# Performance work log

Hardware: AMD Instinct MI355X
Metric: run time of the kernel (lower is better)

Reference implementation:

```python
import math
import jax, jax.numpy as jnp
import numpy as np

B, T, C = 4, 2048, 1024
N_HEAD = 16
HEAD_DIM = C // N_HEAD


def setup_inputs() -> dict:
    key = jax.random.key(0)
    k1, k2, k3 = jax.random.split(key, 3)
    x = jax.random.normal(k1, (B, T, C), dtype=jnp.float32)
    # nn.Linear weights: (out_features, in_features); init scale ~1/sqrt(C)
    w_attn = jax.random.normal(k2, (3 * C, C), dtype=jnp.float32) / math.sqrt(C)
    w_proj = jax.random.normal(k3, (C, C), dtype=jnp.float32) / math.sqrt(C)
    return {"x": x, "w_attn": w_attn, "w_proj": w_proj}


def reference(x, w_attn, w_proj):
    Bx, Tx, Cx = x.shape
    qkv = x @ w_attn.T  # (B,T,3C)
    q, k, v = jnp.split(qkv, 3, axis=2)
    # (B,T,H,D) -> (B,H,T,D)
    q = q.reshape(Bx, Tx, N_HEAD, HEAD_DIM).transpose(0, 2, 1, 3)
    k = k.reshape(Bx, Tx, N_HEAD, HEAD_DIM).transpose(0, 2, 1, 3)
    v = v.reshape(Bx, Tx, N_HEAD, HEAD_DIM).transpose(0, 2, 1, 3)
    scale = 1.0 / math.sqrt(HEAD_DIM)
    att = jnp.einsum("bhqd,bhkd->bhqk", q, k) * scale
    causal = jnp.tril(jnp.ones((Tx, Tx), dtype=bool))
    att = jnp.where(causal[None, None, :, :], att, -jnp.inf)
    att = jax.nn.softmax(att, axis=-1)
    out = jnp.einsum("bhqk,bhkd->bhqd", att, v)
    out = out.transpose(0, 2, 1, 3).reshape(Bx, Tx, Cx)
    return out @ w_proj.T
```

## Files before the change

### kernel.cpp

```cpp
#include <hip/hip_runtime.h>
#include <hip/hip_bf16.h>


typedef __attribute__((ext_vector_type(8))) short bf16x8;
typedef __attribute__((ext_vector_type(4))) float f32x4;
typedef unsigned short ushort_t;

#if __has_builtin(__builtin_amdgcn_exp2f)
#define EXP2(x) __builtin_amdgcn_exp2f(x)
#else
#define EXP2(x) exp2f(x)
#endif

__device__ inline ushort_t f2bf(float f) {
    union { float f; unsigned int u; } x; x.f = f;
    return (ushort_t)((x.u + 0x7fffu + ((x.u >> 16) & 1u)) >> 16);
}

__device__ inline ushort_t f2bf_fast(float f) {
    union { float f; unsigned int u; } x; x.f = f;
    return (ushort_t)((x.u + 0x8000u) >> 16);
}

__device__ inline bf16x8 load8_f32_to_bf16(const float* p) {
    float4 f0 = *(const float4*)p;
    float4 f1 = *(const float4*)(p + 4);
    bf16x8 r;
    r[0] = (short)f2bf(f0.x); r[1] = (short)f2bf(f0.y);
    r[2] = (short)f2bf(f0.z); r[3] = (short)f2bf(f0.w);
    r[4] = (short)f2bf(f1.x); r[5] = (short)f2bf(f1.y);
    r[6] = (short)f2bf(f1.z); r[7] = (short)f2bf(f1.w);
    return r;
}

__device__ inline void gl2lds16(const ushort_t* g, ushort_t* l) {
    __builtin_amdgcn_global_load_lds(
        (const __attribute__((address_space(1))) unsigned int*)g,
        (__attribute__((address_space(3))) unsigned int*)l,
        16, 0, 0);
}

__global__ void cvt3(const float* __restrict__ a, long n8a,
                     const float* __restrict__ b, long n8b,
                     const float* __restrict__ c, long n8c,
                     ushort_t* __restrict__ out) {
    long i = (long)blockIdx.x * 256 + threadIdx.x;
    const float* src; long off;
    if (i < n8a) { src = a; off = i; }
    else if (i < n8a + n8b) { src = b; off = i - n8a; }
    else if (i < n8a + n8b + n8c) { src = c; off = i - n8a - n8b; }
    else return;
    *(bf16x8*)(out + i * 8) = load8_f32_to_bf16(src + off * 8);
}

__global__ void fill_zero_f32(float* out, int n) {
    int i = blockIdx.x * 256 + threadIdx.x;
    if (i < n) out[i] = 0.0f;
}

#define QK_LOG2E_SCALE 0.18033688011112042f

#define OVBUF 16384

template <int EPI>
__global__ __launch_bounds__(256) void gemm_ov(
        const ushort_t* __restrict__ A, const ushort_t* __restrict__ B,
        void* __restrict__ Cp, void* __restrict__ Cp2,
        int M, int N, int K) {
    __shared__ ushort_t S[2 * OVBUF];

    const int tid  = threadIdx.x;
    const int lane = tid & 63;
    const int w    = tid >> 6;
    const int quad = lane >> 4;
    const int l16  = lane & 15;
    const int wm   = (w & 1) * 64;
    const int wn   = (w >> 1) * 64;

    const int xcd = (int)blockIdx.x & 7;
    const int c   = (int)blockIdx.x >> 3;
    const int g   = c >> 6;
    const int ml  = (c >> 3) & 7;
    const int nl  = c & 7;
    const int bm  = ((xcd << 3) + ml) << 7;
    const int bn  = ((g << 3) + nl) << 7;

    const int nt = K >> 6;

    const int srow = lane >> 3;
    const int soct = (lane & 7) ^ srow;
    const ushort_t* Ag = A + (size_t)(bm + w * 32 + srow) * K + soct * 8;
    const ushort_t* Bg = B + (size_t)(bn + w * 32 + srow) * K + soct * 8;

    auto stage = [&](int kt) {
        ushort_t* d = S + (kt & 1) * OVBUF;
        const size_t ko = (size_t)kt * 64;
#pragma unroll
        for (int j = 0; j < 4; j++) {
            gl2lds16(Ag + ko + (size_t)(j * 8) * K, d + w * 2048 + j * 512);
            gl2lds16(Bg + ko + (size_t)(j * 8) * K, d + 8192 + w * 2048 + j * 512);
        }
    };

    const int sl7 = l16 & 7;
    const int ca0 = ((quad)     ^ sl7) * 8;
    const int ca1 = ((quad + 4) ^ sl7) * 8;
    const int arow = (wm + l16) * 64;
    const int brow = 8192 + (wn + l16) * 64;

    f32x4 acc[4][4] = {};

    stage(0);
    __asm__ __volatile__("s_waitcnt vmcnt(0)" ::: "memory");
    __builtin_amdgcn_s_barrier();

    for (int kt = 0; kt < nt; kt++) {
        if (kt + 1 < nt) stage(kt + 1);

        const ushort_t* Sb = S + (kt & 1) * OVBUF;
        bf16x8 af[4][2], bfr[4][2];
#pragma unroll
        for (int mi = 0; mi < 4; mi++) {
            af[mi][0] = *(const bf16x8*)(Sb + arow + mi * 1024 + ca0);
            af[mi][1] = *(const bf16x8*)(Sb + arow + mi * 1024 + ca1);
        }
#pragma unroll
        for (int ni = 0; ni < 4; ni++) {
            bfr[ni][0] = *(const bf16x8*)(Sb + brow + ni * 1024 + ca0);
            bfr[ni][1] = *(const bf16x8*)(Sb + brow + ni * 1024 + ca1);
        }

        __builtin_amdgcn_s_setprio(1);
#pragma unroll
        for (int mi = 0; mi < 4; mi++)
#pragma unroll
            for (int ni = 0; ni < 4; ni++)
#pragma unroll
                for (int kk = 0; kk < 2; kk++)
                    acc[mi][ni] = __builtin_amdgcn_mfma_f32_16x16x32_bf16(
                        af[mi][kk], bfr[ni][kk], acc[mi][ni], 0, 0, 0);
        __builtin_amdgcn_s_setprio(0);

        __asm__ __volatile__("s_waitcnt vmcnt(0)" ::: "memory");
        __builtin_amdgcn_s_barrier();
    }

    const int colbase = bn + wn;
    const int rowbase = bm + wm + quad * 4;
    if constexpr (EPI == 1) {
#pragma unroll
        for (int mi = 0; mi < 4; mi++) {
            const int row = rowbase + mi * 16;
            float* cr = (float*)Cp + (size_t)row * N + colbase + l16;
#pragma unroll
            for (int r = 0; r < 4; r++)
#pragma unroll
                for (int ni = 0; ni < 4; ni++)
                    cr[(size_t)r * N + ni * 16] = acc[mi][ni][r];
        }
    } else {
        if (colbase < 2048) {
            const float qs = (colbase < 1024) ? QK_LOG2E_SCALE : 1.0f;
#pragma unroll
            for (int mi = 0; mi < 4; mi++) {
                const int row = rowbase + mi * 16;
                ushort_t* qp = (ushort_t*)Cp + (size_t)row * 2048 + colbase + l16;
#pragma unroll
                for (int r = 0; r < 4; r++)
#pragma unroll
                    for (int ni = 0; ni < 4; ni++)
                        qp[(size_t)r * 2048 + ni * 16] = f2bf(acc[mi][ni][r] * qs);
            }
        } else {
#pragma unroll
            for (int mi = 0; mi < 4; mi++) {
                const int row = rowbase + mi * 16;
                const int bb = row >> 11, tt = row & 2047;
#pragma unroll
                for (int ni = 0; ni < 4; ni++) {
                    const int vc = colbase + ni * 16 + l16 - 2048;
                    const int hh = vc >> 6, dd = vc & 63;
                    ushort_t* vp = (ushort_t*)Cp2 +
                        ((((size_t)bb * 16 + hh) * 64 + dd) * 2048) + tt;
#pragma unroll
                    for (int r = 0; r < 4; r++)
                        vp[r] = f2bf(acc[mi][ni][r]);
                }
            }
        }
    }
}

#define BM 128
#define BN 128
#define BK 64
#define LDK 72

template <bool A_F32, bool B_F32, int EPI>
__global__ __launch_bounds__(256) void gemm_nt(
        const void* __restrict__ Ap, const void* __restrict__ Bp,
        void* __restrict__ Cp, void* __restrict__ Cp2,
        int M, int N, int K) {
    __shared__ ushort_t As[BM * LDK];
    __shared__ ushort_t Bs[BN * LDK];

    const int tid  = threadIdx.x;
    const int lane = tid & 63;
    const int w    = tid >> 6;
    const int quad = lane >> 4;
    const int l16  = lane & 15;

    const int bm = blockIdx.y * BM;
    const int bn = blockIdx.x * BN;
    const int wm = (w & 1) * 64;
    const int wn = (w >> 1) * 64;

    f32x4 acc[4][4] = {};

    const int lrow = tid >> 3;
    const int lcol = (tid & 7) * 8;

    bf16x8 pa[4], pb[4];
#pragma unroll
    for (int i = 0; i < 4; i++) {
        const int ra = lrow + i * 32;
        if constexpr (A_F32)
            pa[i] = load8_f32_to_bf16((const float*)Ap + (size_t)(bm + ra) * K + lcol);
        else
            pa[i] = *(const bf16x8*)((const ushort_t*)Ap + (size_t)(bm + ra) * K + lcol);
        if constexpr (B_F32)
            pb[i] = load8_f32_to_bf16((const float*)Bp + (size_t)(bn + ra) * K + lcol);
        else
            pb[i] = *(const bf16x8*)((const ushort_t*)Bp + (size_t)(bn + ra) * K + lcol);
    }

    for (int k0 = 0; k0 < K; k0 += BK) {
        __syncthreads();
#pragma unroll
        for (int i = 0; i < 4; i++) {
            *(bf16x8*)&As[(lrow + i * 32) * LDK + lcol] = pa[i];
            *(bf16x8*)&Bs[(lrow + i * 32) * LDK + lcol] = pb[i];
        }
        __syncthreads();

        if (k0 + BK < K) {
            const int kn = k0 + BK + lcol;
#pragma unroll
            for (int i = 0; i < 4; i++) {
                const int ra = lrow + i * 32;
                if constexpr (A_F32)
                    pa[i] = load8_f32_to_bf16((const float*)Ap + (size_t)(bm + ra) * K + kn);
                else
                    pa[i] = *(const bf16x8*)((const ushort_t*)Ap + (size_t)(bm + ra) * K + kn);
                if constexpr (B_F32)
                    pb[i] = load8_f32_to_bf16((const float*)Bp + (size_t)(bn + ra) * K + kn);
                else
                    pb[i] = *(const bf16x8*)((const ushort_t*)Bp + (size_t)(bn + ra) * K + kn);
            }
        }

#pragma unroll
        for (int ks = 0; ks < BK; ks += 32) {
            bf16x8 af[4], bfr[4];
#pragma unroll
            for (int i = 0; i < 4; i++)
                af[i] = *(const bf16x8*)&As[(wm + i * 16 + l16) * LDK + ks + quad * 8];
#pragma unroll
            for (int i = 0; i < 4; i++)
                bfr[i] = *(const bf16x8*)&Bs[(wn + i * 16 + l16) * LDK + ks + quad * 8];
#pragma unroll
            for (int mi = 0; mi < 4; mi++)
#pragma unroll
                for (int ni = 0; ni < 4; ni++)
                    acc[mi][ni] = __builtin_amdgcn_mfma_f32_16x16x32_bf16(
                        af[mi], bfr[ni], acc[mi][ni], 0, 0, 0);
        }
    }

#pragma unroll
    for (int mi = 0; mi < 4; mi++) {
        const int row0 = bm + wm + mi * 16 + quad * 4;
#pragma unroll
        for (int r = 0; r < 4; r++) {
            const int row = row0 + r;
            if constexpr (EPI == 1) {
                float* crow = (float*)Cp + (size_t)row * N + bn + wn;
#pragma unroll
                for (int ni = 0; ni < 4; ni++)
                    crow[ni * 16 + l16] = acc[mi][ni][r];
            } else {
                if (bn < 2048) {
                    const float qs = (bn < 1024) ? QK_LOG2E_SCALE : 1.0f;
                    ushort_t* crow = (ushort_t*)Cp + (size_t)row * 2048 + bn + wn;
#pragma unroll
                    for (int ni = 0; ni < 4; ni++)
                        crow[ni * 16 + l16] = f2bf(acc[mi][ni][r] * qs);
                } else {
                    ushort_t* vt = (ushort_t*)Cp2;
                    const int bb = row >> 11, tt = row & 2047;
#pragma unroll
                    for (int ni = 0; ni < 4; ni++) {
                        const int vc = bn + wn + ni * 16 + l16 - 2048;
                        const int hh = vc >> 6, dd = vc & 63;
                        vt[(((size_t)bb * 16 + hh) * 64 + dd) * 2048 + tt] =
                            f2bf(acc[mi][ni][r]);
                    }
                }
            }
        }
    }
}

#define AT_T 2048

__global__ __launch_bounds__(256) void attn4(
        const ushort_t* __restrict__ qk,
        const ushort_t* __restrict__ vt,
        ushort_t* __restrict__ attout) {
    const int bh   = blockIdx.x;
    const int ya   = (int)blockIdx.y >> 2;
    const int yr   = (int)blockIdx.y & 3;
    const int qblk = (ya == 0) ? 15 - yr
                   : (ya == 1) ? 8 + yr
                   : (ya == 2) ? 4 + yr
                   :             3 - yr;
    const int b    = bh >> 4;
    const int h    = bh & 15;

    const int tid  = threadIdx.x;
    const int lane = tid & 63;
    const int w    = tid >> 6;
    const int quad = lane >> 4;
    const int l16  = lane & 15;
    const int sw   = l16 & 7;

    __shared__ ushort_t Ks[64 * 64];
    __shared__ ushort_t Vs[64 * 64];
    __shared__ ushort_t Ps[4][32 * 64];

    bf16x8 vones;
#pragma unroll
    for (int j = 0; j < 8; j++) vones[j] = (short)0x3F80;

    const ushort_t* qp = qk + (size_t)b * AT_T * 2048 + h * 64;
    const ushort_t* kp = qp + 1024;
    const ushort_t* vp = vt + (size_t)bh * 64 * 2048;

    const int Q0 = qblk * 128 + w * 16;

    bf16x8 aq[2][2];
#pragma unroll
    for (int s = 0; s < 2; s++) {
        const ushort_t* qrow = qp + (size_t)(Q0 + s * 64 + l16) * 2048;
        aq[s][0] = *(const bf16x8*)(qrow + quad * 8);
        aq[s][1] = *(const bf16x8*)(qrow + 32 + quad * 8);
    }

    f32x4 o[2][5] = {};

    const int lr8 = lane >> 3;
    const int cbg = ((lane & 7) ^ lr8) * 8;

    const int nk = 2 * qblk + 2;
    for (int kt = 0; kt < nk; kt++) {
        const int k0 = kt * 64;
        if (kt) __syncthreads();
#pragma unroll
        for (int j = 0; j < 2; j++) {
            gl2lds16(kp + (size_t)(k0 + w * 16 + j * 8 + lr8) * 2048 + cbg,
                     &Ks[(w * 16 + j * 8) * 64]);
            gl2lds16(vp + (size_t)(w * 16 + j * 8 + lr8) * 2048 + k0 + cbg,
                     &Vs[(w * 16 + j * 8) * 64]);
        }
        __syncthreads();

        f32x4 s0[4], s1[4];
#pragma unroll
        for (int c = 0; c < 4; c++) {
            s0[c][0] = -8.0f; s0[c][1] = -8.0f; s0[c][2] = -8.0f; s0[c][3] = -8.0f;
            s1[c] = s0[c];
#pragma unroll
            for (int ks = 0; ks < 2; ks++) {
                const int cs = ((quad + 4 * ks) ^ sw) * 8;
                bf16x8 bk = *(const bf16x8*)&Ks[(c * 16 + l16) * 64 + cs];
                s0[c] = __builtin_amdgcn_mfma_f32_16x16x32_bf16(aq[0][ks], bk, s0[c], 0, 0, 0);
                s1[c] = __builtin_amdgcn_mfma_f32_16x16x32_bf16(aq[1][ks], bk, s1[c], 0, 0, 0);
            }
        }

        if (kt >= 2 * qblk) {
            const int q0r = Q0 + quad * 4;
#pragma unroll
            for (int c = 0; c < 4; c++) {
                const int kcol = k0 + c * 16 + l16;
#pragma unroll
                for (int r = 0; r < 4; r++)
                    if (kcol > q0r + r) s0[c][r] = -__builtin_inff();
            }
        }
        if (kt == 2 * qblk + 1) {
            const int q1r = Q0 + 64 + quad * 4;
#pragma unroll
            for (int c = 0; c < 4; c++) {
                const int kcol = k0 + c * 16 + l16;
#pragma unroll
                for (int r = 0; r < 4; r++)
                    if (kcol > q1r + r) s1[c][r] = -__builtin_inff();
            }
        }

#pragma unroll
        for (int c = 0; c < 4; c++)
#pragma unroll
            for (int r = 0; r < 4; r++) {
                const int row = quad * 4 + r;
                const int sidx = (((c * 2 + (l16 >> 3)) ^ (row & 7)) << 3) | sw;
                Ps[w][row * 64 + sidx]        = f2bf_fast(EXP2(s0[c][r]));
                Ps[w][(16 + row) * 64 + sidx] = f2bf_fast(EXP2(s1[c][r]));
            }

        __asm__ __volatile__("s_waitcnt lgkmcnt(0)" ::: "memory");

#pragma unroll
        for (int ks = 0; ks < 2; ks++) {
            const int cs = ((quad + 4 * ks) ^ sw) * 8;
            const int pslot = (((ks * 4 + quad) ^ sw) << 3);
            bf16x8 ap0 = *(const bf16x8*)&Ps[w][l16 * 64 + pslot];
            bf16x8 ap1 = *(const bf16x8*)&Ps[w][(16 + l16) * 64 + pslot];
#pragma unroll
            for (int n = 0; n < 4; n++) {
                bf16x8 bv = *(const bf16x8*)&Vs[(n * 16 + l16) * 64 + cs];
                o[0][n] = __builtin_amdgcn_mfma_f32_16x16x32_bf16(ap0, bv, o[0][n], 0, 0, 0);
                o[1][n] = __builtin_amdgcn_mfma_f32_16x16x32_bf16(ap1, bv, o[1][n], 0, 0, 0);
            }
            o[0][4] = __builtin_amdgcn_mfma_f32_16x16x32_bf16(ap0, vones, o[0][4], 0, 0, 0);
            o[1][4] = __builtin_amdgcn_mfma_f32_16x16x32_bf16(ap1, vones, o[1][4], 0, 0, 0);
        }
    }

#pragma unroll
    for (int s = 0; s < 2; s++) {
        ushort_t* op = attout + (size_t)(b * AT_T + Q0 + s * 64 + quad * 4) * 1024 + h * 64;
#pragma unroll
        for (int r = 0; r < 4; r++) {
            const float l = __shfl(o[s][4][r], lane & 48, 64);
            const float inv = 1.0f / fmaxf(l, 1e-30f);
            ushort_t* orow = op + (size_t)r * 1024;
#pragma unroll
            for (int n = 0; n < 4; n++)
                orow[n * 16 + l16] = f2bf(o[s][n][r] * inv);
        }
    }
}

extern "C" void kernel_launch(void* const* d_in, const int* in_sizes, int n_in,
                              void* d_out, int out_size, void* d_ws, size_t ws_size,
                              hipStream_t stream) {
    const float* x      = (const float*)d_in[0];
    const float* w_attn = (const float*)d_in[1];
    const float* w_proj = (const float*)d_in[2];
    float* out = (float*)d_out;

    const int M = 8192, C = 1024;
    const size_t E_QK  = (size_t)M * 2048;
    const size_t E_VT  = (size_t)4 * 16 * 64 * 2048;
    const size_t E_ATT = (size_t)M * 1024;
    const size_t E_X   = (size_t)M * 1024;
    const size_t E_WA  = (size_t)3072 * 1024;
    const size_t E_WP  = (size_t)1024 * 1024;
    const size_t need_mid  = (E_QK + E_VT + E_ATT) * 2;
    const size_t need_full = need_mid + (E_X + E_WA + E_WP) * 2;

    if (ws_size < need_mid) {
        fill_zero_f32<<<(out_size + 255) / 256, 256, 0, stream>>>(out, out_size);
        return;
    }

    ushort_t* qk  = (ushort_t*)d_ws;
    ushort_t* vt  = qk + E_QK;
    ushort_t* att = vt + E_VT;

    if (ws_size >= need_full) {
        ushort_t* xb  = att + E_ATT;
        const long n8x = (long)(E_X / 8), n8a = (long)(E_WA / 8), n8p = (long)(E_WP / 8);
        const long n8  = n8x + n8a + n8p;
        cvt3<<<(int)((n8 + 255) / 256), 256, 0, stream>>>(
            x, n8x, w_attn, n8a, w_proj, n8p, xb);

        ushort_t* wab = xb + E_X;
        ushort_t* wpb = wab + E_WA;
        gemm_ov<2><<<dim3((M / 128) * (3 * C / 128)), 256, 0, stream>>>(
            xb, wab, qk, vt, M, 3 * C, C);
        attn4<<<dim3(64, 16), 256, 0, stream>>>(qk, vt, att);
        gemm_ov<1><<<dim3((M / 128) * (C / 128)), 256, 0, stream>>>(
            att, wpb, out, nullptr, M, C, C);
    } else {
        gemm_nt<true, true, 2><<<dim3(3 * C / BN, M / BM), 256, 0, stream>>>(
            x, w_attn, qk, vt, M, 3 * C, C);
        attn4<<<dim3(64, 16), 256, 0, stream>>>(qk, vt, att);
        gemm_nt<false, true, 1><<<dim3(C / BN, M / BM), 256, 0, stream>>>(
            att, w_proj, out, nullptr, M, C, C);
    }
}
```

Baseline: 225.8 us.

## Halve attention query tile to 64 rows and transpose score MFMA for packed P stores

The attention kernel now handles 64 query rows per block instead of 128, so each wave owns 16 rows and the grid doubles to 32 query blocks per head, and the block order becomes simple longest-first. The QK^T MFMA swaps its operands so each lane holds 4 consecutive key columns, which lets the P tile be written to LDS as packed 64-bit stores instead of scalar 16-bit stores. The causal mask now applies only on the single diagonal tile. This cuts LDS store instructions and register pressure and allows more blocks to be resident, but each K/V tile loaded into LDS is now reused by half as many query rows, doubling K/V traffic.

```diff
diff --git a/kernel.cpp b/kernel.cpp
--- a/kernel.cpp
+++ b/kernel.cpp
@@ -20,6 +20,10 @@
 __device__ inline ushort_t f2bf_fast(float f) {
     union { float f; unsigned int u; } x; x.f = f;
     return (ushort_t)((x.u + 0x8000u) >> 16);
+}
+
+__device__ inline unsigned int pk2(float lo, float hi) {
+    return (unsigned int)f2bf_fast(lo) | ((unsigned int)f2bf_fast(hi) << 16);
 }
 
 __device__ inline bf16x8 load8_f32_to_bf16(const float* p) {
@@ -318,12 +322,7 @@
         const ushort_t* __restrict__ vt,
         ushort_t* __restrict__ attout) {
     const int bh   = blockIdx.x;
-    const int ya   = (int)blockIdx.y >> 2;
-    const int yr   = (int)blockIdx.y & 3;
-    const int qblk = (ya == 0) ? 15 - yr
-                   : (ya == 1) ? 8 + yr
-                   : (ya == 2) ? 4 + yr
-                   :             3 - yr;
+    const int qblk = (gridDim.y - 1) - blockIdx.y;
     const int b    = bh >> 4;
     const int h    = bh & 15;
 
@@ -336,7 +335,7 @@
 
     __shared__ ushort_t Ks[64 * 64];
     __shared__ ushort_t Vs[64 * 64];
-    __shared__ ushort_t Ps[4][32 * 64];
+    __shared__ ushort_t Ps[4][16 * 64];
 
     bf16x8 vones;
 #pragma unroll
@@ -346,22 +345,21 @@
     const ushort_t* kp = qp + 1024;
     const ushort_t* vp = vt + (size_t)bh * 64 * 2048;
 
-    const int Q0 = qblk * 128 + w * 16;
-
-    bf16x8 aq[2][2];
-#pragma unroll
-    for (int s = 0; s < 2; s++) {
-        const ushort_t* qrow = qp + (size_t)(Q0 + s * 64 + l16) * 2048;
-        aq[s][0] = *(const bf16x8*)(qrow + quad * 8);
-        aq[s][1] = *(const bf16x8*)(qrow + 32 + quad * 8);
-    }
-
-    f32x4 o[2][5] = {};
+    const int Q0 = qblk * 64 + w * 16;
+
+    bf16x8 aq[2];
+    {
+        const ushort_t* qrow = qp + (size_t)(Q0 + l16) * 2048;
+        aq[0] = *(const bf16x8*)(qrow + quad * 8);
+        aq[1] = *(const bf16x8*)(qrow + 32 + quad * 8);
+    }
+
+    f32x4 o[5] = {};
 
     const int lr8 = lane >> 3;
     const int cbg = ((lane & 7) ^ lr8) * 8;
 
-    const int nk = 2 * qblk + 2;
+    const int nk = qblk + 1;
     for (int kt = 0; kt < nk; kt++) {
         const int k0 = kt * 64;
         if (kt) __syncthreads();
@@ -374,82 +372,64 @@
         }
         __syncthreads();
 
-        f32x4 s0[4], s1[4];
+        f32x4 s0[4];
 #pragma unroll
         for (int c = 0; c < 4; c++) {
             s0[c][0] = -8.0f; s0[c][1] = -8.0f; s0[c][2] = -8.0f; s0[c][3] = -8.0f;
-            s1[c] = s0[c];
 #pragma unroll
             for (int ks = 0; ks < 2; ks++) {
                 const int cs = ((quad + 4 * ks) ^ sw) * 8;
                 bf16x8 bk = *(const bf16x8*)&Ks[(c * 16 + l16) * 64 + cs];
-                s0[c] = __builtin_amdgcn_mfma_f32_16x16x32_bf16(aq[0][ks], bk, s0[c], 0, 0, 0);
-                s1[c] = __builtin_amdgcn_mfma_f32_16x16x32_bf16(aq[1][ks], bk, s1[c], 0, 0, 0);
-            }
-        }
-
-        if (kt >= 2 * qblk) {
-            const int q0r = Q0 + quad * 4;
+                s0[c] = __builtin_amdgcn_mfma_f32_16x16x32_bf16(bk, aq[ks], s0[c], 0, 0, 0);
+            }
+        }
+
+        if (kt == qblk) {
+            const int ql = w * 16 + l16;
 #pragma unroll
             for (int c = 0; c < 4; c++) {
-                const int kcol = k0 + c * 16 + l16;
+                const int kb = c * 16 + quad * 4;
 #pragma unroll
                 for (int r = 0; r < 4; r++)
-                    if (kcol > q0r + r) s0[c][r] = -__builtin_inff();
-            }
-        }
-        if (kt == 2 * qblk + 1) {
-            const int q1r = Q0 + 64 + quad * 4;
-#pragma unroll
-            for (int c = 0; c < 4; c++) {
-                const int kcol = k0 + c * 16 + l16;
-#pragma unroll
-                for (int r = 0; r < 4; r++)
-                    if (kcol > q1r + r) s1[c][r] = -__builtin_inff();
-            }
-        }
-
-#pragma unroll
-        for (int c = 0; c < 4; c++)
-#pragma unroll
-            for (int r = 0; r < 4; r++) {
-                const int row = quad * 4 + r;
-                const int sidx = (((c * 2 + (l16 >> 3)) ^ (row & 7)) << 3) | sw;
-                Ps[w][row * 64 + sidx]        = f2bf_fast(EXP2(s0[c][r]));
-                Ps[w][(16 + row) * 64 + sidx] = f2bf_fast(EXP2(s1[c][r]));
-            }
+                    if (kb + r > ql) s0[c][r] = -__builtin_inff();
+            }
+        }
+
+#pragma unroll
+        for (int c = 0; c < 4; c++) {
+            const int g = quad + 4 * c;
+            const int off = (((g >> 1) ^ sw) << 3) + ((g & 1) << 2);
+            uint2 wv;
+            wv.x = pk2(EXP2(s0[c][0]), EXP2(s0[c][1]));
+            wv.y = pk2(EXP2(s0[c][2]), EXP2(s0[c][3]));
+            *(uint2*)&Ps[w][l16 * 64 + off] = wv;
+        }
 
         __asm__ __volatile__("s_waitcnt lgkmcnt(0)" ::: "memory");
 
 #pragma unroll
         for (int ks = 0; ks < 2; ks++) {
             const int cs = ((quad + 4 * ks) ^ sw) * 8;
-            const int pslot = (((ks * 4 + quad) ^ sw) << 3);
-            bf16x8 ap0 = *(const bf16x8*)&Ps[w][l16 * 64 + pslot];
-            bf16x8 ap1 = *(const bf16x8*)&Ps[w][(16 + l16) * 64 + pslot];
+            const int po = (((ks * 4 + quad) ^ sw) << 3);
+            bf16x8 ap = *(const bf16x8*)&Ps[w][l16 * 64 + po];
 #pragma unroll
             for (int n = 0; n < 4; n++) {
                 bf16x8 bv = *(const bf16x8*)&Vs[(n * 16 + l16) * 64 + cs];
-                o[0][n] = __builtin_amdgcn_mfma_f32_16x16x32_bf16(ap0, bv, o[0][n], 0, 0, 0);
-                o[1][n] = __builtin_amdgcn_mfma_f32_16x16x32_bf16(ap1, bv, o[1][n], 0, 0, 0);
-            }
-            o[0][4] = __builtin_amdgcn_mfma_f32_16x16x32_bf16(ap0, vones, o[0][4], 0, 0, 0);
-            o[1][4] = __builtin_amdgcn_mfma_f32_16x16x32_bf16(ap1, vones, o[1][4], 0, 0, 0);
-        }
-    }
-
-#pragma unroll
-    for (int s = 0; s < 2; s++) {
-        ushort_t* op = attout + (size_t)(b * AT_T + Q0 + s * 64 + quad * 4) * 1024 + h * 64;
-#pragma unroll
-        for (int r = 0; r < 4; r++) {
-            const float l = __shfl(o[s][4][r], lane & 48, 64);
-            const float inv = 1.0f / fmaxf(l, 1e-30f);
-            ushort_t* orow = op + (size_t)r * 1024;
-#pragma unroll
-            for (int n = 0; n < 4; n++)
-                orow[n * 16 + l16] = f2bf(o[s][n][r] * inv);
-        }
+                o[n] = __builtin_amdgcn_mfma_f32_16x16x32_bf16(ap, bv, o[n], 0, 0, 0);
+            }
+            o[4] = __builtin_amdgcn_mfma_f32_16x16x32_bf16(ap, vones, o[4], 0, 0, 0);
+        }
+    }
+
+    ushort_t* op = attout + (size_t)(b * AT_T + Q0 + quad * 4) * 1024 + h * 64;
+#pragma unroll
+    for (int r = 0; r < 4; r++) {
+        const float l = __shfl(o[4][r], lane & 48, 64);
+        const float inv = 1.0f / fmaxf(l, 1e-30f);
+        ushort_t* orow = op + (size_t)r * 1024;
+#pragma unroll
+        for (int n = 0; n < 4; n++)
+            orow[n * 16 + l16] = f2bf(o[n][r] * inv);
     }
 }
 
@@ -491,13 +471,13 @@
         ushort_t* wpb = wab + E_WA;
         gemm_ov<2><<<dim3((M / 128) * (3 * C / 128)), 256, 0, stream>>>(
             xb, wab, qk, vt, M, 3 * C, C);
-        attn4<<<dim3(64, 16), 256, 0, stream>>>(qk, vt, att);
+        attn4<<<dim3(64, 32), 256, 0, stream>>>(qk, vt, att);
         gemm_ov<1><<<dim3((M / 128) * (C / 128)), 256, 0, stream>>>(
             att, wpb, out, nullptr, M, C, C);
     } else {
         gemm_nt<true, true, 2><<<dim3(3 * C / BN, M / BM), 256, 0, stream>>>(
             x, w_attn, qk, vt, M, 3 * C, C);
-        attn4<<<dim3(64, 16), 256, 0, stream>>>(qk, vt, att);
+        attn4<<<dim3(64, 32), 256, 0, stream>>>(qk, vt, att);
         gemm_nt<false, true, 1><<<dim3(C / BN, M / BM), 256, 0, stream>>>(
             att, w_proj, out, nullptr, M, C, C);
     }
```

Result: no change. 221.9 us (-1.8%).
